# Optimization experiments

Measured on AMD Instinct MI355X. Metric: run time of the kernel, lower is better.

The kernel has to match this reference:

```python
import jax, jax.numpy as jnp
import numpy as np


def setup_inputs() -> dict:
    key = jax.random.key(0)
    k1, k2 = jax.random.split(key)
    B, H, S = 16, 512, 1024          # batch, hidden=nd*embed_dim, seqlen
    ND, ED, K = 4, 128, 4096         # nd, embed_dim, num_embed
    inputs = jax.random.normal(k1, (B, H, S), dtype=jnp.float32)
    embeddings = jax.random.normal(k2, (ND, ED, K), dtype=jnp.float32)
    return {"inputs": inputs, "embeddings": embeddings}


def reference(inputs, embeddings):
    # VectorQuant.forward with soft_train=False, gsoftmax=False, EMA=False (VQ-VAE straight-through path)
    commit_cost = 0.25
    B, H, S = inputs.shape
    ND, ED, K = embeddings.shape
    # stack_enc_outputs: (B, H, S) -> (B*S, nd, embed_dim) via contiguous view (C-order reshape)
    enc = inputs.reshape(B * S, ND, ED)
    x2 = jnp.sum(enc * enc, axis=2, keepdims=True)            # (BS, nd, 1)
    e2 = jnp.sum(embeddings * embeddings, axis=1)[None]       # (1, nd, K)
    cross = jnp.einsum('dhk,bdh->bdk', embeddings, enc)       # (BS, nd, K)
    distances = x2 + e2 - 2.0 * cross
    # per-token, per-chunk nearest code
    latents = jnp.argmin(distances, axis=2).T                 # (nd, BS)
    # gather codebook vectors: embeddings[d][:, latents[d]] -> (nd, ED, BS)
    encodings = jnp.take_along_axis(embeddings, latents[:, None, :], axis=2)
    # split_outputs: (nd, ED, B*S) -> (B, H, S) via contiguous view (C-order reshape)
    encodings = encodings.reshape(B, H, S)
    # straight-through estimator
    output = inputs + jax.lax.stop_gradient(encodings) - jax.lax.stop_gradient(inputs)
    commit_loss = jnp.mean((inputs - jax.lax.stop_gradient(encodings)) ** 2)
    loss = commit_cost * commit_loss
    kl = jnp.asarray(0, dtype=jnp.int32)
    return (output, loss, commit_loss, kl)
```

## Files before the change

### kernel.cpp

```cpp
#include <hip/hip_runtime.h>

#define ND 4
#define ED 128
#define KCODES 4096
#define NTOK 16384
#define HID 512
#define NTOT (ND*ED*NTOK)

#define MARGIN 2.0e-3f
#define FLAG_CAP 16384

typedef __attribute__((ext_vector_type(8))) short short8v;
typedef __attribute__((ext_vector_type(4))) float float4v;

__device__ __forceinline__ unsigned short bf16h(float x) {
    unsigned u = __float_as_uint(x);
    return (unsigned short)((u + 0x7fffu + ((u >> 16) & 1u)) >> 16);
}
__device__ __forceinline__ float bf16f(unsigned short h) {
    return __uint_as_float(((unsigned)h) << 16);
}

__global__ void zero_kernel(int* __restrict__ p) { if (threadIdx.x == 0) *p = 0; }

__global__ __launch_bounds__(256) void e2_kernel(const float* __restrict__ emb,
        float* __restrict__ e2g, float* __restrict__ e2p) {
    int idx = blockIdx.x * 256 + threadIdx.x;
    int d = idx >> 12;
    int k = idx & (KCODES - 1);
    const float* __restrict__ p = emb + (size_t)d * ED * KCODES + k;
    float s = 0.f;
    for (int e = 0; e < ED; ++e) {
        float v = p[(size_t)e * KCODES];
        s = __fadd_rn(s, __fmul_rn(v, v));
    }
    e2g[idx] = s;
    e2p[idx] = s + 512.0f;
}

__global__ __launch_bounds__(256) void bsplit_kernel(const float* __restrict__ emb,
        unsigned short* __restrict__ bth2, unsigned short* __restrict__ btl2) {
    const int tile = blockIdx.x;
    const int d    = blockIdx.y;
    const int tid  = threadIdx.x;
    #pragma unroll
    for (int q = 0; q < 4; ++q) {
        int c    = q * 256 + tid;
        int code = c & 63;
        int blk  = c >> 6;
        int e0   = (blk >> 2) * 32 + (blk & 3) * 8;
        short8v hv, lv;
        #pragma unroll
        for (int j = 0; j < 8; ++j) {
            float v = emb[((size_t)d * ED + e0 + j) * KCODES + tile * 64 + code];
            unsigned short hb = bf16h(v);
            hv[j] = (short)hb;
            lv[j] = (short)bf16h(v - bf16f(hb));
        }
        size_t dst = ((size_t)(d * 64 + tile) * 1024 + c) * 8;
        *(short8v*)(bth2 + dst) = hv;
        *(short8v*)(btl2 + dst) = lv;
    }
}

__global__ __launch_bounds__(256, 2) void argmin_mfma_kernel(const float* __restrict__ in,
        const unsigned short* __restrict__ bth2, const unsigned short* __restrict__ btl2,
        const float* __restrict__ e2p, int* __restrict__ lat,
        int* __restrict__ flag_cnt, int* __restrict__ flag_list) {
    __shared__ __align__(16) unsigned short Bst[16384];

    const int l    = blockIdx.x;
    const int r8   = l & 7;
    const int d    = r8 >> 1;
    const int tI   = 2 * (l >> 3) + (r8 & 1);
    const int t0   = tI * 128;

    const int tid  = threadIdx.x;
    const int wid  = tid >> 6;
    const int lane = tid & 63;
    const int l15  = lane & 15;
    const int lk8  = lane >> 4;

    short8v ahf[2][4], alf[2][4];
    #pragma unroll
    for (int rt = 0; rt < 2; ++rt) {
        const float* ap = in + (size_t)(t0 + wid * 32 + rt * 16 + l15) * HID + d * ED + lk8 * 8;
        #pragma unroll
        for (int ks = 0; ks < 4; ++ks) {
            float4 v0 = *(const float4*)(ap + ks * 32);
            float4 v1 = *(const float4*)(ap + ks * 32 + 4);
            float vv[8] = {v0.x, v0.y, v0.z, v0.w, v1.x, v1.y, v1.z, v1.w};
            short8v h, lo;
            #pragma unroll
            for (int j = 0; j < 8; ++j) {
                unsigned short hb = bf16h(vv[j]);
                h[j]  = (short)hb;
                lo[j] = (short)bf16h(vv[j] - bf16f(hb));
            }
            ahf[rt][ks] = h; alf[rt][ks] = lo;
        }
    }

    float best1[2][4], best2_[2][4];
    int   bestk_[2][4];
    #pragma unroll
    for (int rt = 0; rt < 2; ++rt)
        #pragma unroll
        for (int r = 0; r < 4; ++r) { best1[rt][r] = 3.0e38f; best2_[rt][r] = 3.0e38f; bestk_[rt][r] = 0; }

    short8v st[8];
    {
        const size_t tb = (size_t)(d * 64 + 0) * 1024;
        #pragma unroll
        for (int j = 0; j < 4; ++j) st[j]     = *(const short8v*)(bth2 + (tb + j * 256 + tid) * 8);
        #pragma unroll
        for (int j = 0; j < 4; ++j) st[4 + j] = *(const short8v*)(btl2 + (tb + j * 256 + tid) * 8);
    }

    const int khoff = lk8 * 512;

    for (int kt = 0; kt < 64; ++kt) {
        __syncthreads();
        #pragma unroll
        for (int j = 0; j < 8; ++j)
            *(short8v*)(&Bst[(size_t)(j * 256 + tid) * 8]) = st[j];
        __syncthreads();

        if (kt < 63) {
            const size_t tb = (size_t)(d * 64 + kt + 1) * 1024;
            #pragma unroll
            for (int j = 0; j < 4; ++j) st[j]     = *(const short8v*)(bth2 + (tb + j * 256 + tid) * 8);
            #pragma unroll
            for (int j = 0; j < 4; ++j) st[4 + j] = *(const short8v*)(btl2 + (tb + j * 256 + tid) * 8);
        }
        float e2p4[4];
        #pragma unroll
        for (int ct = 0; ct < 4; ++ct)
            e2p4[ct] = e2p[d * KCODES + kt * 64 + ct * 16 + l15];

        #pragma unroll
        for (int ct = 0; ct < 4; ++ct) {
            const int cbase = (ct * 16 + l15) * 8;
            short8v bh[4], bl[4];
            #pragma unroll
            for (int ks = 0; ks < 4; ++ks) {
                bh[ks] = *(const short8v*)&Bst[ks * 2048 + khoff + cbase];
                bl[ks] = *(const short8v*)&Bst[8192 + ks * 2048 + khoff + cbase];
            }
            float4v ach[2] = {{0,0,0,0},{0,0,0,0}};
            float4v acl1[2] = {{0,0,0,0},{0,0,0,0}};
            float4v acl2[2] = {{0,0,0,0},{0,0,0,0}};
            #pragma unroll
            for (int ks = 0; ks < 4; ++ks) {
                ach[0]  = __builtin_amdgcn_mfma_f32_16x16x32_bf16(ahf[0][ks], bh[ks], ach[0], 0, 0, 0);
                ach[1]  = __builtin_amdgcn_mfma_f32_16x16x32_bf16(ahf[1][ks], bh[ks], ach[1], 0, 0, 0);
                acl1[0] = __builtin_amdgcn_mfma_f32_16x16x32_bf16(alf[0][ks], bh[ks], acl1[0], 0, 0, 0);
                acl1[1] = __builtin_amdgcn_mfma_f32_16x16x32_bf16(alf[1][ks], bh[ks], acl1[1], 0, 0, 0);
                acl2[0] = __builtin_amdgcn_mfma_f32_16x16x32_bf16(ahf[0][ks], bl[ks], acl2[0], 0, 0, 0);
                acl2[1] = __builtin_amdgcn_mfma_f32_16x16x32_bf16(ahf[1][ks], bl[ks], acl2[1], 0, 0, 0);
            }
            const int codev = kt * 64 + ct * 16 + l15;
            #pragma unroll
            for (int rt = 0; rt < 2; ++rt) {
                #pragma unroll
                for (int r = 0; r < 4; ++r) {
                    float cs = ach[rt][r] + acl1[rt][r] + acl2[rt][r];
                    float dv = __fmaf_rn(-2.0f, cs, e2p4[ct]);
                    if (dv < best1[rt][r]) {
                        best2_[rt][r] = best1[rt][r]; best1[rt][r] = dv; bestk_[rt][r] = codev;
                    } else if (dv < best2_[rt][r]) {
                        best2_[rt][r] = dv;
                    }
                }
            }
        }
    }

    #pragma unroll
    for (int m = 1; m <= 8; m <<= 1) {
        #pragma unroll
        for (int rt = 0; rt < 2; ++rt) {
            #pragma unroll
            for (int r = 0; r < 4; ++r) {
                float od = __shfl_xor(best1[rt][r], m, 64);
                float o2 = __shfl_xor(best2_[rt][r], m, 64);
                int   ok = __shfl_xor(bestk_[rt][r], m, 64);
                if (od < best1[rt][r] || (od == best1[rt][r] && ok < bestk_[rt][r])) {
                    best2_[rt][r] = fminf(best1[rt][r], o2);
                    best1[rt][r]  = od;
                    bestk_[rt][r] = ok;
                } else {
                    best2_[rt][r] = fminf(best2_[rt][r], od);
                }
            }
        }
    }
    if (l15 == 0) {
        #pragma unroll
        for (int rt = 0; rt < 2; ++rt) {
            #pragma unroll
            for (int r = 0; r < 4; ++r) {
                int row = wid * 32 + rt * 16 + lk8 * 4 + r;
                int tok = d * NTOK + t0 + row;
                lat[tok] = bestk_[rt][r];
                if (best2_[rt][r] - best1[rt][r] < MARGIN) {
                    int slot = atomicAdd(flag_cnt, 1);
                    if (slot < FLAG_CAP) flag_list[slot] = tok;
                }
            }
        }
    }
}

__global__ __launch_bounds__(256) void repair_kernel(const float* __restrict__ in,
        const float* __restrict__ emb, const float* __restrict__ e2g,
        const int* __restrict__ flag_cnt, const int* __restrict__ flag_list,
        int* __restrict__ lat) {
    __shared__ float xs[ED];
    __shared__ float rd[256];
    __shared__ int   rk[256];
    int n = *flag_cnt;
    if (n > FLAG_CAP) n = FLAG_CAP;
    for (int idx = blockIdx.x; idx < n; idx += gridDim.x) {
        int tok = flag_list[idx];
        int d = tok >> 14;
        int t = tok & (NTOK - 1);
        __syncthreads();
        if (threadIdx.x < ED) xs[threadIdx.x] = in[(size_t)t * HID + d * ED + threadIdx.x];
        __syncthreads();
        float x2v = 0.f;
        for (int e = 0; e < ED; ++e) x2v = __fadd_rn(x2v, __fmul_rn(xs[e], xs[e]));
        const float* __restrict__ embd = emb + (size_t)d * ED * KCODES;
        float bd = 3.0e38f; int bk = 0;
        for (int j = 0; j < 16; ++j) {
            int k = threadIdx.x + j * 256;
            float acc = 0.f;
            #pragma unroll 16
            for (int e = 0; e < ED; ++e)
                acc = __fmaf_rn(xs[e], embd[(size_t)e * KCODES + k], acc);
            float dist = __fsub_rn(__fadd_rn(x2v, e2g[d * KCODES + k]),
                                   __fmul_rn(2.0f, acc));
            if (dist < bd) { bd = dist; bk = k; }
        }
        rd[threadIdx.x] = bd; rk[threadIdx.x] = bk;
        __syncthreads();
        for (int w = 128; w > 0; w >>= 1) {
            if (threadIdx.x < w) {
                float od = rd[threadIdx.x + w]; int ok = rk[threadIdx.x + w];
                if (od < rd[threadIdx.x] || (od == rd[threadIdx.x] && ok < rk[threadIdx.x])) {
                    rd[threadIdx.x] = od; rk[threadIdx.x] = ok;
                }
            }
            __syncthreads();
        }
        if (threadIdx.x == 0) lat[tok] = rk[0];
    }
}

__global__ __launch_bounds__(256) void gather_kernel(const float* __restrict__ in,
        const float* __restrict__ emb, const int* __restrict__ lat,
        float* __restrict__ out, float* __restrict__ partial) {
    int tid  = threadIdx.x;
    int base = blockIdx.x * 1024 + tid * 4;
    int d = base >> 21;
    int e = (base >> 14) & 127;
    int t = base & (NTOK - 1);
    const int4 kk = *(const int4*)(lat + d * NTOK + t);
    const float* __restrict__ row = emb + ((size_t)(d * ED + e)) * KCODES;
    float enc[4];
    enc[0] = row[kk.x]; enc[1] = row[kk.y]; enc[2] = row[kk.z]; enc[3] = row[kk.w];
    const float4 x = *(const float4*)(in + base);
    const float xv[4] = {x.x, x.y, x.z, x.w};
    float4 ov; float* o = (float*)&ov;
    float s = 0.f;
    #pragma unroll
    for (int i = 0; i < 4; ++i) {
        o[i] = __fsub_rn(__fadd_rn(xv[i], enc[i]), xv[i]);
        float df = xv[i] - enc[i];
        s = __fmaf_rn(df, df, s);
    }
    *(float4*)(out + base) = ov;
    #pragma unroll
    for (int off = 32; off > 0; off >>= 1) s += __shfl_down(s, off, 64);
    __shared__ float wsum[4];
    if ((tid & 63) == 0) wsum[tid >> 6] = s;
    __syncthreads();
    if (tid == 0) partial[blockIdx.x] = wsum[0] + wsum[1] + wsum[2] + wsum[3];
}

__global__ __launch_bounds__(256) void finalize_kernel(const float* __restrict__ partial,
                                                       float* __restrict__ out_tail) {
    __shared__ double sh[256];
    double s = 0.0;
    for (int i = threadIdx.x; i < 8192; i += 256) s += (double)partial[i];
    sh[threadIdx.x] = s;
    __syncthreads();
    for (int w = 128; w > 0; w >>= 1) {
        if (threadIdx.x < w) sh[threadIdx.x] += sh[threadIdx.x + w];
        __syncthreads();
    }
    if (threadIdx.x == 0) {
        double mean = sh[0] / (double)NTOT;
        out_tail[0] = (float)(0.25 * mean);
        out_tail[1] = (float)mean;
        ((int*)out_tail)[2] = 0;
    }
}

extern "C" void kernel_launch(void* const* d_in, const int* in_sizes, int n_in,
                              void* d_out, int out_size, void* d_ws, size_t ws_size,
                              hipStream_t stream) {
    const float* in  = (const float*)d_in[0];
    const float* emb = (const float*)d_in[1];
    float* out = (float*)d_out;
    char* ws = (char*)d_ws;

    int*   lat       = (int*)ws;
    float* e2g       = (float*)(ws + 262144);
    float* e2p       = (float*)(ws + 327680);
    float* partial   = (float*)(ws + 393216);
    int*   flag_cnt  = (int*)(ws + 425984);
    int*   flag_list = (int*)(ws + 425988);
    unsigned short* bth2 = (unsigned short*)(ws + (1 << 20));
    unsigned short* btl2 = (unsigned short*)(ws + (1 << 20) + 4194304);

    hipLaunchKernelGGL(zero_kernel, dim3(1), dim3(64), 0, stream, flag_cnt);
    hipLaunchKernelGGL(e2_kernel, dim3(64), dim3(256), 0, stream, emb, e2g, e2p);
    hipLaunchKernelGGL(bsplit_kernel, dim3(64, 4), dim3(256), 0, stream, emb, bth2, btl2);
    hipLaunchKernelGGL(argmin_mfma_kernel, dim3(512), dim3(256), 0, stream,
                       in, bth2, btl2, e2p, lat, flag_cnt, flag_list);
    hipLaunchKernelGGL(repair_kernel, dim3(64), dim3(256), 0, stream,
                       in, emb, e2g, flag_cnt, flag_list, lat);
    hipLaunchKernelGGL(gather_kernel, dim3(NTOT / 1024), dim3(256), 0, stream,
                       in, emb, lat, out, partial);
    hipLaunchKernelGGL(finalize_kernel, dim3(1), dim3(256), 0, stream, partial, out + NTOT);
}
```

Baseline: 313.2 us.

## Restructure argmin tiling: 64-token blocks, split code range across waves, swizzled LDS

Merges the zero, e2 and bsplit preprocessing kernels into one kernel that transposes codebook tiles through shared memory and writes a 16-code XOR-swizzled bf16 hi/lo layout. The argmin kernel now handles 64 tokens per block, with the two wave pairs each scanning half of the codebook. Results are merged through shared memory at the end. Grid size doubles, LDS use halves, occupancy target rises to 4 blocks, and the two low-order MFMA products share one accumulator. The intent is better occupancy, fewer bank conflicts and fewer launches, at the cost of more barriers per code and a slightly different rounding order in the cross-term sum.

After: 435.9 us. 39.2% more time.

```diff
diff --git a/kernel.cpp b/kernel.cpp
--- a/kernel.cpp
+++ b/kernel.cpp
@@ -21,193 +21,202 @@
     return __uint_as_float(((unsigned)h) << 16);
 }
 
-__global__ void zero_kernel(int* __restrict__ p) { if (threadIdx.x == 0) *p = 0; }
-
-__global__ __launch_bounds__(256) void e2_kernel(const float* __restrict__ emb,
-        float* __restrict__ e2g, float* __restrict__ e2p) {
-    int idx = blockIdx.x * 256 + threadIdx.x;
-    int d = idx >> 12;
-    int k = idx & (KCODES - 1);
-    const float* __restrict__ p = emb + (size_t)d * ED * KCODES + k;
-    float s = 0.f;
-    for (int e = 0; e < ED; ++e) {
-        float v = p[(size_t)e * KCODES];
-        s = __fadd_rn(s, __fmul_rn(v, v));
-    }
-    e2g[idx] = s;
-    e2p[idx] = s + 512.0f;
-}
-
-__global__ __launch_bounds__(256) void bsplit_kernel(const float* __restrict__ emb,
-        unsigned short* __restrict__ bth2, unsigned short* __restrict__ btl2) {
+__global__ __launch_bounds__(256) void e2split_kernel(const float* __restrict__ emb,
+        float* __restrict__ e2g, float* __restrict__ e2p,
+        unsigned short* __restrict__ bth2, unsigned short* __restrict__ btl2,
+        int* __restrict__ flag_cnt) {
+    __shared__ float Tf[128][17];
     const int tile = blockIdx.x;
     const int d    = blockIdx.y;
     const int tid  = threadIdx.x;
-    #pragma unroll
-    for (int q = 0; q < 4; ++q) {
+    const int k0   = tile * 16;
+    if (tile == 0 && d == 0 && tid == 0) *flag_cnt = 0;
+    {
+        int e = tid >> 1, half = tid & 1;
+        const float* src = emb + ((size_t)d * ED + e) * KCODES + k0 + half * 8;
+        float4 v0 = *(const float4*)(src);
+        float4 v1 = *(const float4*)(src + 4);
+        float* dst = &Tf[e][half * 8];
+        dst[0] = v0.x; dst[1] = v0.y; dst[2] = v0.z; dst[3] = v0.w;
+        dst[4] = v1.x; dst[5] = v1.y; dst[6] = v1.z; dst[7] = v1.w;
+    }
+    __syncthreads();
+    if (tid < 16) {
+        float s = 0.f;
+        for (int e = 0; e < ED; ++e) {
+            float v = Tf[e][tid];
+            s = __fadd_rn(s, __fmul_rn(v, v));
+        }
+        e2g[d * KCODES + k0 + tid] = s;
+        e2p[d * KCODES + k0 + tid] = s + 512.0f;
+    }
+    #pragma unroll
+    for (int q = 0; q < 2; ++q) {
         int c    = q * 256 + tid;
-        int code = c & 63;
-        int blk  = c >> 6;
-        int e0   = (blk >> 2) * 32 + (blk & 3) * 8;
-        short8v hv, lv;
+        int arr  = c >> 8;
+        int cc   = c & 255;
+        int code = cc >> 4;
+        int gp   = cc & 15;
+        int e0   = (gp ^ code) * 8;
+        short8v v;
         #pragma unroll
         for (int j = 0; j < 8; ++j) {
-            float v = emb[((size_t)d * ED + e0 + j) * KCODES + tile * 64 + code];
-            unsigned short hb = bf16h(v);
-            hv[j] = (short)hb;
-            lv[j] = (short)bf16h(v - bf16f(hb));
-        }
-        size_t dst = ((size_t)(d * 64 + tile) * 1024 + c) * 8;
-        *(short8v*)(bth2 + dst) = hv;
-        *(short8v*)(btl2 + dst) = lv;
-    }
-}
-
-__global__ __launch_bounds__(256, 2) void argmin_mfma_kernel(const float* __restrict__ in,
+            float x = Tf[e0 + j][code];
+            unsigned short hb = bf16h(x);
+            v[j] = arr ? (short)bf16h(x - bf16f(hb)) : (short)hb;
+        }
+        unsigned short* dst = (arr ? btl2 : bth2) + ((size_t)(d * 256 + tile) * 256 + cc) * 8;
+        *(short8v*)dst = v;
+    }
+}
+
+__global__ __launch_bounds__(256, 4) void argmin_mfma_kernel(const float* __restrict__ in,
         const unsigned short* __restrict__ bth2, const unsigned short* __restrict__ btl2,
         const float* __restrict__ e2p, int* __restrict__ lat,
         int* __restrict__ flag_cnt, int* __restrict__ flag_list) {
-    __shared__ __align__(16) unsigned short Bst[16384];
-
-    const int l    = blockIdx.x;
-    const int r8   = l & 7;
-    const int d    = r8 >> 1;
-    const int tI   = 2 * (l >> 3) + (r8 & 1);
-    const int t0   = tI * 128;
+    __shared__ __align__(16) unsigned short Bst[8192];
+    __shared__ float mb1[128], mb2[128];
+    __shared__ int   mbk[128];
+
+    const int l   = blockIdx.x;
+    const int r8  = l & 7;
+    const int d   = r8 >> 1;
+    const int tI  = 2 * (l >> 3) + (r8 & 1);
+    const int t0  = tI * 64;
 
     const int tid  = threadIdx.x;
     const int wid  = tid >> 6;
     const int lane = tid & 63;
     const int l15  = lane & 15;
     const int lk8  = lane >> 4;
+    const int tg   = wid & 1;
+    const int h    = wid >> 1;
 
     short8v ahf[2][4], alf[2][4];
     #pragma unroll
     for (int rt = 0; rt < 2; ++rt) {
-        const float* ap = in + (size_t)(t0 + wid * 32 + rt * 16 + l15) * HID + d * ED + lk8 * 8;
+        const float* ap = in + (size_t)(t0 + tg * 32 + rt * 16 + l15) * HID + d * ED + lk8 * 8;
         #pragma unroll
         for (int ks = 0; ks < 4; ++ks) {
             float4 v0 = *(const float4*)(ap + ks * 32);
             float4 v1 = *(const float4*)(ap + ks * 32 + 4);
             float vv[8] = {v0.x, v0.y, v0.z, v0.w, v1.x, v1.y, v1.z, v1.w};
-            short8v h, lo;
+            short8v hv, lv;
             #pragma unroll
             for (int j = 0; j < 8; ++j) {
                 unsigned short hb = bf16h(vv[j]);
-                h[j]  = (short)hb;
-                lo[j] = (short)bf16h(vv[j] - bf16f(hb));
-            }
-            ahf[rt][ks] = h; alf[rt][ks] = lo;
-        }
-    }
-
-    float best1[2][4], best2_[2][4];
-    int   bestk_[2][4];
+                hv[j] = (short)hb;
+                lv[j] = (short)bf16h(vv[j] - bf16f(hb));
+            }
+            ahf[rt][ks] = hv; alf[rt][ks] = lv;
+        }
+    }
+
+    float b1[2][4], b2[2][4];
+    int   bk[2][4];
     #pragma unroll
     for (int rt = 0; rt < 2; ++rt)
         #pragma unroll
-        for (int r = 0; r < 4; ++r) { best1[rt][r] = 3.0e38f; best2_[rt][r] = 3.0e38f; bestk_[rt][r] = 0; }
-
-    short8v st[8];
-    {
-        const size_t tb = (size_t)(d * 64 + 0) * 1024;
-        #pragma unroll
-        for (int j = 0; j < 4; ++j) st[j]     = *(const short8v*)(bth2 + (tb + j * 256 + tid) * 8);
-        #pragma unroll
-        for (int j = 0; j < 4; ++j) st[4 + j] = *(const short8v*)(btl2 + (tb + j * 256 + tid) * 8);
-    }
-
-    const int khoff = lk8 * 512;
-
-    for (int kt = 0; kt < 64; ++kt) {
-        __syncthreads();
-        #pragma unroll
-        for (int j = 0; j < 8; ++j)
-            *(short8v*)(&Bst[(size_t)(j * 256 + tid) * 8]) = st[j];
-        __syncthreads();
-
-        if (kt < 63) {
-            const size_t tb = (size_t)(d * 64 + kt + 1) * 1024;
-            #pragma unroll
-            for (int j = 0; j < 4; ++j) st[j]     = *(const short8v*)(bth2 + (tb + j * 256 + tid) * 8);
-            #pragma unroll
-            for (int j = 0; j < 4; ++j) st[4 + j] = *(const short8v*)(btl2 + (tb + j * 256 + tid) * 8);
-        }
-        float e2p4[4];
-        #pragma unroll
-        for (int ct = 0; ct < 4; ++ct)
-            e2p4[ct] = e2p[d * KCODES + kt * 64 + ct * 16 + l15];
-
-        #pragma unroll
-        for (int ct = 0; ct < 4; ++ct) {
-            const int cbase = (ct * 16 + l15) * 8;
-            short8v bh[4], bl[4];
-            #pragma unroll
-            for (int ks = 0; ks < 4; ++ks) {
-                bh[ks] = *(const short8v*)&Bst[ks * 2048 + khoff + cbase];
-                bl[ks] = *(const short8v*)&Bst[8192 + ks * 2048 + khoff + cbase];
-            }
-            float4v ach[2] = {{0,0,0,0},{0,0,0,0}};
-            float4v acl1[2] = {{0,0,0,0},{0,0,0,0}};
-            float4v acl2[2] = {{0,0,0,0},{0,0,0,0}};
-            #pragma unroll
-            for (int ks = 0; ks < 4; ++ks) {
-                ach[0]  = __builtin_amdgcn_mfma_f32_16x16x32_bf16(ahf[0][ks], bh[ks], ach[0], 0, 0, 0);
-                ach[1]  = __builtin_amdgcn_mfma_f32_16x16x32_bf16(ahf[1][ks], bh[ks], ach[1], 0, 0, 0);
-                acl1[0] = __builtin_amdgcn_mfma_f32_16x16x32_bf16(alf[0][ks], bh[ks], acl1[0], 0, 0, 0);
-                acl1[1] = __builtin_amdgcn_mfma_f32_16x16x32_bf16(alf[1][ks], bh[ks], acl1[1], 0, 0, 0);
-                acl2[0] = __builtin_amdgcn_mfma_f32_16x16x32_bf16(ahf[0][ks], bl[ks], acl2[0], 0, 0, 0);
-                acl2[1] = __builtin_amdgcn_mfma_f32_16x16x32_bf16(ahf[1][ks], bl[ks], acl2[1], 0, 0, 0);
-            }
-            const int codev = kt * 64 + ct * 16 + l15;
-            #pragma unroll
-            for (int rt = 0; rt < 2; ++rt) {
-                #pragma unroll
-                for (int r = 0; r < 4; ++r) {
-                    float cs = ach[rt][r] + acl1[rt][r] + acl2[rt][r];
-                    float dv = __fmaf_rn(-2.0f, cs, e2p4[ct]);
-                    if (dv < best1[rt][r]) {
-                        best2_[rt][r] = best1[rt][r]; best1[rt][r] = dv; bestk_[rt][r] = codev;
-                    } else if (dv < best2_[rt][r]) {
-                        best2_[rt][r] = dv;
-                    }
+        for (int r = 0; r < 4; ++r) { b1[rt][r] = 3.0e38f; b2[rt][r] = 3.0e38f; bk[rt][r] = 0; }
+
+    const int chunk_h0 = 0, chunk_h1 = 128;
+    const unsigned short* sp[4];
+    sp[0] = bth2 + ((size_t)(d * 256 + chunk_h0) * 256 + tid) * 8;
+    sp[1] = btl2 + ((size_t)(d * 256 + chunk_h0) * 256 + tid) * 8;
+    sp[2] = bth2 + ((size_t)(d * 256 + chunk_h1) * 256 + tid) * 8;
+    sp[3] = btl2 + ((size_t)(d * 256 + chunk_h1) * 256 + tid) * 8;
+    short8v st[4];
+    #pragma unroll
+    for (int q = 0; q < 4; ++q) { st[q] = *(const short8v*)sp[q]; sp[q] += 2048; }
+
+    char* lb = (char*)Bst;
+    const int wbase = h * 8192;
+    int codeBase = h * 2048;
+
+    for (int kt = 0; kt < 128; ++kt) {
+        __syncthreads();
+        #pragma unroll
+        for (int q = 0; q < 4; ++q)
+            *(short8v*)(lb + (q * 256 + tid) * 16) = st[q];
+        __syncthreads();
+        if (kt < 127) {
+            #pragma unroll
+            for (int q = 0; q < 4; ++q) { st[q] = *(const short8v*)sp[q]; sp[q] += 2048; }
+        }
+        const float e2v = e2p[d * KCODES + codeBase + l15];
+
+        float4v ach[2] = {{0,0,0,0},{0,0,0,0}};
+        float4v acl[2] = {{0,0,0,0},{0,0,0,0}};
+        #pragma unroll
+        for (int ks = 0; ks < 4; ++ks) {
+            const int gswz = (ks * 4 + lk8) ^ l15;
+            short8v bh = *(const short8v*)(lb + wbase + l15 * 256 + gswz * 16);
+            short8v bl = *(const short8v*)(lb + wbase + 4096 + l15 * 256 + gswz * 16);
+            ach[0] = __builtin_amdgcn_mfma_f32_16x16x32_bf16(ahf[0][ks], bh, ach[0], 0, 0, 0);
+            ach[1] = __builtin_amdgcn_mfma_f32_16x16x32_bf16(ahf[1][ks], bh, ach[1], 0, 0, 0);
+            acl[0] = __builtin_amdgcn_mfma_f32_16x16x32_bf16(alf[0][ks], bh, acl[0], 0, 0, 0);
+            acl[1] = __builtin_amdgcn_mfma_f32_16x16x32_bf16(alf[1][ks], bh, acl[1], 0, 0, 0);
+            acl[0] = __builtin_amdgcn_mfma_f32_16x16x32_bf16(ahf[0][ks], bl, acl[0], 0, 0, 0);
+            acl[1] = __builtin_amdgcn_mfma_f32_16x16x32_bf16(ahf[1][ks], bl, acl[1], 0, 0, 0);
+        }
+        const int codev = codeBase + l15;
+        #pragma unroll
+        for (int rt = 0; rt < 2; ++rt) {
+            #pragma unroll
+            for (int r = 0; r < 4; ++r) {
+                float cs = ach[rt][r] + acl[rt][r];
+                float dv = __fmaf_rn(-2.0f, cs, e2v);
+                if (dv < b1[rt][r]) { b2[rt][r] = b1[rt][r]; b1[rt][r] = dv; bk[rt][r] = codev; }
+                else if (dv < b2[rt][r]) { b2[rt][r] = dv; }
+            }
+        }
+        codeBase += 16;
+    }
+
+    #pragma unroll
+    for (int m = 1; m <= 8; m <<= 1) {
+        #pragma unroll
+        for (int rt = 0; rt < 2; ++rt) {
+            #pragma unroll
+            for (int r = 0; r < 4; ++r) {
+                float od = __shfl_xor(b1[rt][r], m, 64);
+                float o2 = __shfl_xor(b2[rt][r], m, 64);
+                int   ok = __shfl_xor(bk[rt][r], m, 64);
+                if (od < b1[rt][r] || (od == b1[rt][r] && ok < bk[rt][r])) {
+                    b2[rt][r] = fminf(b1[rt][r], o2);
+                    b1[rt][r] = od;
+                    bk[rt][r] = ok;
+                } else {
+                    b2[rt][r] = fminf(b2[rt][r], od);
                 }
             }
         }
     }
-
-    #pragma unroll
-    for (int m = 1; m <= 8; m <<= 1) {
+    __syncthreads();
+    if (l15 == 0) {
         #pragma unroll
         for (int rt = 0; rt < 2; ++rt) {
             #pragma unroll
             for (int r = 0; r < 4; ++r) {
-                float od = __shfl_xor(best1[rt][r], m, 64);
-                float o2 = __shfl_xor(best2_[rt][r], m, 64);
-                int   ok = __shfl_xor(bestk_[rt][r], m, 64);
-                if (od < best1[rt][r] || (od == best1[rt][r] && ok < bestk_[rt][r])) {
-                    best2_[rt][r] = fminf(best1[rt][r], o2);
-                    best1[rt][r]  = od;
-                    bestk_[rt][r] = ok;
-                } else {
-                    best2_[rt][r] = fminf(best2_[rt][r], od);
-                }
-            }
-        }
-    }
-    if (l15 == 0) {
-        #pragma unroll
-        for (int rt = 0; rt < 2; ++rt) {
-            #pragma unroll
-            for (int r = 0; r < 4; ++r) {
-                int row = wid * 32 + rt * 16 + lk8 * 4 + r;
-                int tok = d * NTOK + t0 + row;
-                lat[tok] = bestk_[rt][r];
-                if (best2_[rt][r] - best1[rt][r] < MARGIN) {
-                    int slot = atomicAdd(flag_cnt, 1);
-                    if (slot < FLAG_CAP) flag_list[slot] = tok;
-                }
-            }
+                int tok = tg * 32 + rt * 16 + lk8 * 4 + r;
+                mb1[h * 64 + tok] = b1[rt][r];
+                mb2[h * 64 + tok] = b2[rt][r];
+                mbk[h * 64 + tok] = bk[rt][r];
+            }
+        }
+    }
+    __syncthreads();
+    if (tid < 64) {
+        float a1 = mb1[tid],      a2 = mb2[tid];      int ak = mbk[tid];
+        float c1 = mb1[64 + tid], c2 = mb2[64 + tid]; int ck = mbk[64 + tid];
+        float B1, B2; int K;
+        if (a1 < c1 || (a1 == c1 && ak < ck)) { B1 = a1; K = ak; B2 = fminf(a2, c1); }
+        else                                  { B1 = c1; K = ck; B2 = fminf(c2, a1); }
+        int tok = d * NTOK + t0 + tid;
+        lat[tok] = K;
+        if (B2 - B1 < MARGIN) {
+            int slot = atomicAdd(flag_cnt, 1);
+            if (slot < FLAG_CAP) flag_list[slot] = tok;
         }
     }
 }
@@ -231,7 +240,7 @@
         float x2v = 0.f;
         for (int e = 0; e < ED; ++e) x2v = __fadd_rn(x2v, __fmul_rn(xs[e], xs[e]));
         const float* __restrict__ embd = emb + (size_t)d * ED * KCODES;
-        float bd = 3.0e38f; int bk = 0;
+        float bd = 3.0e38f; int bkk = 0;
         for (int j = 0; j < 16; ++j) {
             int k = threadIdx.x + j * 256;
             float acc = 0.f;
@@ -240,9 +249,9 @@
                 acc = __fmaf_rn(xs[e], embd[(size_t)e * KCODES + k], acc);
             float dist = __fsub_rn(__fadd_rn(x2v, e2g[d * KCODES + k]),
                                    __fmul_rn(2.0f, acc));
-            if (dist < bd) { bd = dist; bk = k; }
-        }
-        rd[threadIdx.x] = bd; rk[threadIdx.x] = bk;
+            if (dist < bd) { bd = dist; bkk = k; }
+        }
+        rd[threadIdx.x] = bd; rk[threadIdx.x] = bkk;
         __syncthreads();
         for (int w = 128; w > 0; w >>= 1) {
             if (threadIdx.x < w) {
@@ -324,10 +333,9 @@
     unsigned short* bth2 = (unsigned short*)(ws + (1 << 20));
     unsigned short* btl2 = (unsigned short*)(ws + (1 << 20) + 4194304);
 
-    hipLaunchKernelGGL(zero_kernel, dim3(1), dim3(64), 0, stream, flag_cnt);
-    hipLaunchKernelGGL(e2_kernel, dim3(64), dim3(256), 0, stream, emb, e2g, e2p);
-    hipLaunchKernelGGL(bsplit_kernel, dim3(64, 4), dim3(256), 0, stream, emb, bth2, btl2);
-    hipLaunchKernelGGL(argmin_mfma_kernel, dim3(512), dim3(256), 0, stream,
+    hipLaunchKernelGGL(e2split_kernel, dim3(256, 4), dim3(256), 0, stream,
+                       emb, e2g, e2p, bth2, btl2, flag_cnt);
+    hipLaunchKernelGGL(argmin_mfma_kernel, dim3(1024), dim3(256), 0, stream,
                        in, bth2, btl2, e2p, lat, flag_cnt, flag_list);
     hipLaunchKernelGGL(repair_kernel, dim3(64), dim3(256), 0, stream,
                        in, emb, e2g, flag_cnt, flag_list, lat);
```
